# Optimization experiments

Measured on AMD Instinct MI355X. Metric: run time of the kernel, lower is better.

The kernel has to match this reference:

```python
import jax, jax.numpy as jnp
import numpy as np

B, N_IN, N_H, N_OUT = 128, 256, 256, 256


def _bimul(W, X):
    # MatrixBiMul: bilinear map W X W^T, W: [out, in], X: [b, in, in] -> [b, out, out]
    return jnp.einsum('oi,bij,qj->boq', W, X, W)


def setup_inputs() -> dict:
    key = jax.random.key(0)
    ks = jax.random.split(key, 12)
    s_in = 1.0 / np.sqrt(N_IN)
    s_h = 1.0 / np.sqrt(N_H)
    return {
        'input': jax.random.normal(ks[0], (B, N_IN, N_IN), jnp.float32),
        'hidden': jax.random.normal(ks[1], (B, N_H, N_H), jnp.float32),
        'cell': jax.random.normal(ks[2], (B, N_H, N_H), jnp.float32),
        'W_fx': jax.random.normal(ks[3], (N_H, N_IN), jnp.float32) * s_in,
        'W_ix': jax.random.normal(ks[4], (N_H, N_IN), jnp.float32) * s_in,
        'W_ox': jax.random.normal(ks[5], (N_OUT, N_IN), jnp.float32) * s_in,
        'W_gx': jax.random.normal(ks[6], (N_H, N_IN), jnp.float32) * s_in,
        'W_fh': jax.random.normal(ks[7], (N_H, N_H), jnp.float32) * s_h,
        'W_ih': jax.random.normal(ks[8], (N_H, N_H), jnp.float32) * s_h,
        'W_oh': jax.random.normal(ks[9], (N_OUT, N_H), jnp.float32) * s_h,
        'W_gh': jax.random.normal(ks[10], (N_H, N_H), jnp.float32) * s_h,
        'W_oc': jax.random.normal(ks[11], (N_OUT, N_H), jnp.float32) * s_h,
    }


def reference(input, hidden, cell, W_fx, W_ix, W_ox, W_gx, W_fh, W_ih, W_oh, W_gh, W_oc):
    fgate = jax.nn.relu(_bimul(W_fx, input) + _bimul(W_fh, hidden))
    igate = jax.nn.relu(_bimul(W_ix, input) + _bimul(W_ih, hidden))
    ogate = jax.nn.relu(_bimul(W_ox, input) + _bimul(W_oh, hidden))
    ggate = jax.nn.relu(_bimul(W_gx, input) + _bimul(W_gh, hidden))
    c = fgate + cell + igate + ggate  # note: additive, as in source (not fgate*cell)
    h = ogate + jax.nn.relu(_bimul(W_oc, c))
    return (h, c)
```

## Files before the change

### kernel.cpp

```cpp
#include <hip/hip_runtime.h>

typedef __bf16 bf16x8 __attribute__((ext_vector_type(8)));
typedef float f32x4 __attribute__((ext_vector_type(4)));

__device__ __forceinline__ unsigned short f2bf(float f) {
    unsigned int u = __builtin_bit_cast(unsigned int, f);
    u += 0x7fff + ((u >> 16) & 1);
    return (unsigned short)(u >> 16);
}

__device__ __forceinline__ void stage_pair(
    const unsigned short* __restrict__ Ap, int lda,
    const unsigned short* __restrict__ Bp, int ldb,
    unsigned short* lds, int k0, int tid)
{
#pragma unroll
    for (int it = 0; it < 4; ++it) {
        int li = it * 256 + tid;
        int row = li >> 3;
        int sc = ((li & 7) ^ (row & 7)) * 8;
        __builtin_amdgcn_global_load_lds(
            (const __attribute__((address_space(1))) void*)(Ap + (long)row * lda + k0 + sc),
            (__attribute__((address_space(3))) void*)&lds[li * 8], 16, 0, 0);
        __builtin_amdgcn_global_load_lds(
            (const __attribute__((address_space(1))) void*)(Bp + (long)row * ldb + k0 + sc),
            (__attribute__((address_space(3))) void*)&lds[8192 + li * 8], 16, 0, 0);
    }
}

__device__ __forceinline__ void stage_one(
    const unsigned short* __restrict__ Ap, int lda,
    unsigned short* buf, int k0, int tid)
{
#pragma unroll
    for (int it = 0; it < 4; ++it) {
        int li = it * 256 + tid;
        int row = li >> 3;
        int sc = ((li & 7) ^ (row & 7)) * 8;
        __builtin_amdgcn_global_load_lds(
            (const __attribute__((address_space(1))) void*)(Ap + (long)row * lda + k0 + sc),
            (__attribute__((address_space(3))) void*)&buf[li * 8], 16, 0, 0);
    }
}

__device__ __forceinline__ void compute_tile(
    const unsigned short* lds, int lane, int wm, int wn, f32x4 (&acc)[4][4])
{
#pragma unroll
    for (int kk = 0; kk < 2; ++kk) {
        const int cl = kk * 4 + (lane >> 4);
        bf16x8 af[4], bfr[4];
#pragma unroll
        for (int m = 0; m < 4; ++m) {
            int row = wm + m * 16 + (lane & 15);
            af[m] = *(const bf16x8*)&lds[row * 64 + ((cl ^ (row & 7)) * 8)];
        }
#pragma unroll
        for (int n = 0; n < 4; ++n) {
            int row = wn + n * 16 + (lane & 15);
            bfr[n] = *(const bf16x8*)&lds[8192 + row * 64 + ((cl ^ (row & 7)) * 8)];
        }
#pragma unroll
        for (int m = 0; m < 4; ++m)
#pragma unroll
            for (int n = 0; n < 4; ++n)
                acc[m][n] = __builtin_amdgcn_mfma_f32_16x16x32_bf16(af[m], bfr[n], acc[m][n], 0, 0, 0);
    }
}

__device__ __forceinline__ void compute_bsc(
    const unsigned short* bufA, const unsigned short* Sc, int k0,
    int lane, int wm, int wn, f32x4 (&acc)[4][4])
{
#pragma unroll
    for (int kk = 0; kk < 2; ++kk) {
        const int cl = kk * 4 + (lane >> 4);
        bf16x8 af[4], bfr[4];
#pragma unroll
        for (int m = 0; m < 4; ++m) {
            int row = wm + m * 16 + (lane & 15);
            af[m] = *(const bf16x8*)&bufA[row * 64 + ((cl ^ (row & 7)) * 8)];
        }
#pragma unroll
        for (int n = 0; n < 4; ++n) {
            int row = wn + n * 16 + (lane & 15);
            bfr[n] = *(const bf16x8*)&Sc[row * 256 + k0 + ((cl ^ (row & 7)) * 8)];
        }
#pragma unroll
        for (int m = 0; m < 4; ++m)
#pragma unroll
            for (int n = 0; n < 4; ++n)
                acc[m][n] = __builtin_amdgcn_mfma_f32_16x16x32_bf16(af[m], bfr[n], acc[m][n], 0, 0, 0);
    }
}

__global__ __launch_bounds__(256)
void cvt_all(const float* __restrict__ X, const float* __restrict__ H,
             unsigned short* __restrict__ XHb,
             const float* __restrict__ fx, const float* __restrict__ ix,
             const float* __restrict__ ox, const float* __restrict__ gx,
             const float* __restrict__ fh, const float* __restrict__ ih,
             const float* __restrict__ oh, const float* __restrict__ gh,
             const float* __restrict__ oc,
             unsigned short* __restrict__ Wcat, unsigned short* __restrict__ Wocb)
{
    int bid = blockIdx.x;
    if (bid < 8192) {
        long e = ((long)bid * 256 + threadIdx.x) * 8;
        const float* s = (e < 8388608) ? (X + e) : (H + (e - 8388608));
        float4 a = *(const float4*)s;
        float4 c = *(const float4*)(s + 4);
        uint4 uv;
        uv.x = (unsigned)f2bf(a.x) | ((unsigned)f2bf(a.y) << 16);
        uv.y = (unsigned)f2bf(a.z) | ((unsigned)f2bf(a.w) << 16);
        uv.z = (unsigned)f2bf(c.x) | ((unsigned)f2bf(c.y) << 16);
        uv.w = (unsigned)f2bf(c.z) | ((unsigned)f2bf(c.w) << 16);
        *(uint4*)&XHb[e] = uv;
    } else {
        int idx = (bid - 8192) * 256 + threadIdx.x;
        if (idx < 524288) {
            int g = idx >> 17;
            int rem = idx & 131071;
            int q = rem >> 9;
            int j = rem & 511;
            const float* xs = (g == 0) ? fx : (g == 1) ? ix : (g == 2) ? ox : gx;
            const float* hs = (g == 0) ? fh : (g == 1) ? ih : (g == 2) ? oh : gh;
            float v = (j < 256) ? xs[q * 256 + j] : hs[q * 256 + (j - 256)];
            Wcat[idx] = f2bf(v);
        } else if (idx < 589824) {
            int k = idx - 524288;
            Wocb[k] = f2bf(oc[k]);
        }
    }
}

__global__ __launch_bounds__(256)
void gemm_s1(const unsigned short* __restrict__ Wcat,
             const unsigned short* __restrict__ XHb,
             unsigned short* __restrict__ Tcat)
{
    __shared__ alignas(16) unsigned short lds[16384];

    const int tid = threadIdx.x;
    const int lane = tid & 63;
    const int w = tid >> 6;

    int d = blockIdx.x + 4 * blockIdx.y + 512 * blockIdx.z;
    int swz = (d & 7) * 512 + (d >> 3);
    const int x = swz & 3;
    const int b = (swz >> 2) & 127;
    const int gz = swz >> 9;
    const int g = gz >> 1, hf = gz & 1;
    const int tq = (x >> 1) * 128;
    const int ti = (x & 1) * 128;
    const int wm = (w >> 1) * 64;
    const int wn = (w & 1) * 64;

    const unsigned short* Ap = Wcat + (long)g * 131072 + (long)tq * 512 + hf * 256;
    const unsigned short* Bp = XHb + (long)hf * 8388608 + (long)b * 65536 + (long)ti * 256;

    f32x4 acc[4][4];
#pragma unroll
    for (int m = 0; m < 4; ++m)
#pragma unroll
        for (int n = 0; n < 4; ++n)
            acc[m][n] = (f32x4){0.f, 0.f, 0.f, 0.f};

#pragma unroll
    for (int t = 0; t < 4; ++t) {
        if (t > 0) __syncthreads();
        stage_pair(Ap, 512, Bp, 256, lds, t * 64, tid);
        __syncthreads();
        compute_tile(lds, lane, wm, wn, acc);
    }

    unsigned short* Cb = Tcat + (long)g * 16777216 + (long)b * 131072 + hf * 256;
    const int r0 = (lane >> 4) * 4;
    const int c0 = lane & 15;
#pragma unroll
    for (int m = 0; m < 4; ++m)
#pragma unroll
        for (int n = 0; n < 4; ++n)
#pragma unroll
            for (int r = 0; r < 4; ++r) {
                int row = tq + wm + m * 16 + r0 + r;
                int col = ti + wn + n * 16 + c0;
                Cb[(long)row * 512 + col] = f2bf(acc[m][n][r]);
            }
}

__global__ __launch_bounds__(256)
void gemm_gateB(const unsigned short* __restrict__ Tcat,
                const unsigned short* __restrict__ Wcat,
                const float* __restrict__ cell,
                float* __restrict__ out_c, float* __restrict__ out_h,
                unsigned short* __restrict__ cb16)
{
    __shared__ alignas(16) unsigned short lds[32768];

    const int tid = threadIdx.x;
    const int lane = tid & 63;
    const int w = tid >> 6;

    int orig = blockIdx.x + 4 * blockIdx.y;
    int swz = (orig & 7) * 64 + (orig >> 3);
    const int x = swz & 3;
    const int b = swz >> 2;
    const int to = (x >> 1) * 128;
    const int tq = (x & 1) * 128;
    const int wm = (w >> 1) * 64;
    const int wn = (w & 1) * 64;

    f32x4 accc[4][4], acc[4][4];
#pragma unroll
    for (int m = 0; m < 4; ++m)
#pragma unroll
        for (int n = 0; n < 4; ++n) {
            accc[m][n] = (f32x4){0.f, 0.f, 0.f, 0.f};
            acc[m][n] = (f32x4){0.f, 0.f, 0.f, 0.f};
        }

    {
        const unsigned short* Ap0 = Wcat + (long)to * 512;
        const unsigned short* Bp0 = Tcat + (long)b * 131072 + (long)tq * 512;
        stage_pair(Ap0, 512, Bp0, 512, lds, 0, tid);
    }
    for (int u = 0; u < 32; ++u) {
        __syncthreads();
        if (u + 1 < 32) {
            int s = (u + 1) >> 3;
            int gv = s ^ (s >> 1);
            const unsigned short* Ap = Wcat + (long)gv * 131072 + (long)to * 512;
            const unsigned short* Bp = Tcat + (long)gv * 16777216 + (long)b * 131072 + (long)tq * 512;
            stage_pair(Ap, 512, Bp, 512, lds + ((u + 1) & 1) * 16384, ((u + 1) & 7) * 64, tid);
        }
        compute_tile(lds + (u & 1) * 16384, lane, wm, wn, acc);
        if ((u & 7) == 7 && u != 31) {
#pragma unroll
            for (int m = 0; m < 4; ++m)
#pragma unroll
                for (int n = 0; n < 4; ++n)
#pragma unroll
                    for (int r = 0; r < 4; ++r) {
                        float v = acc[m][n][r];
                        accc[m][n][r] += (v > 0.f ? v : 0.f);
                        acc[m][n][r] = 0.f;
                    }
        }
    }

    const float* cb = cell + (long)b * 65536;
    float* co = out_c + (long)b * 65536;
    float* ho = out_h + (long)b * 65536;
    unsigned short* cbo = cb16 + (long)b * 65536;
    const int r0 = (lane >> 4) * 4;
    const int c0 = lane & 15;
#pragma unroll
    for (int m = 0; m < 4; ++m)
#pragma unroll
        for (int n = 0; n < 4; ++n)
#pragma unroll
            for (int r = 0; r < 4; ++r) {
                int row = to + wm + m * 16 + r0 + r;
                int col = tq + wn + n * 16 + c0;
                long idx = (long)row * 256 + col;
                float cv = accc[m][n][r] + cb[idx];
                co[idx] = cv;
                cbo[idx] = f2bf(cv);
                float v = acc[m][n][r];
                ho[idx] = (v > 0.f ? v : 0.f);
            }
}

__global__ __launch_bounds__(256)
void gemm_woc(const unsigned short* __restrict__ Wocb,
              const unsigned short* __restrict__ cb16,
              float* __restrict__ out_h)
{
    __shared__ alignas(16) unsigned short stg[32768];
    __shared__ alignas(16) unsigned short Sc[32768];

    const int tid = threadIdx.x;
    const int lane = tid & 63;
    const int w = tid >> 6;

    int orig = blockIdx.x + 2 * blockIdx.y;
    int swz = (orig & 7) * 32 + (orig >> 3);
    const int b = swz >> 1;
    const int tq = (swz & 1) * 128;
    const int wm = (w >> 1) * 64;
    const int wn = (w & 1) * 64;
    const int r0 = (lane >> 4) * 4;
    const int c0 = lane & 15;

#pragma unroll
    for (int t2 = 0; t2 < 2; ++t2) {
        const unsigned short* Ap = Wocb + (long)tq * 256;
        const unsigned short* Bp = cb16 + (long)b * 65536 + (long)(t2 * 128) * 256;

        f32x4 acc[4][4];
#pragma unroll
        for (int m = 0; m < 4; ++m)
#pragma unroll
            for (int n = 0; n < 4; ++n)
                acc[m][n] = (f32x4){0.f, 0.f, 0.f, 0.f};

        stage_pair(Ap, 256, Bp, 256, stg, 0, tid);
#pragma unroll
        for (int t = 0; t < 4; ++t) {
            __syncthreads();
            if (t + 1 < 4)
                stage_pair(Ap, 256, Bp, 256, stg + ((t + 1) & 1) * 16384, (t + 1) * 64, tid);
            compute_tile(stg + (t & 1) * 16384, lane, wm, wn, acc);
        }
#pragma unroll
        for (int m = 0; m < 4; ++m)
#pragma unroll
            for (int n = 0; n < 4; ++n)
#pragma unroll
                for (int r = 0; r < 4; ++r) {
                    int qrow = wm + m * 16 + r0 + r;
                    int icol = t2 * 128 + wn + n * 16 + c0;
                    int addr = qrow * 256 + (icol & ~63)
                             + ((((icol >> 3) & 7) ^ (qrow & 7)) * 8) + (icol & 7);
                    Sc[addr] = f2bf(acc[m][n][r]);
                }
    }

    float* ho = out_h + (long)b * 65536;
#pragma unroll
    for (int ot = 0; ot < 2; ++ot) {
        const unsigned short* Ap = Wocb + (long)(ot * 128) * 256;

        f32x4 acc[4][4];
#pragma unroll
        for (int m = 0; m < 4; ++m)
#pragma unroll
            for (int n = 0; n < 4; ++n)
                acc[m][n] = (f32x4){0.f, 0.f, 0.f, 0.f};

        stage_one(Ap, 256, stg, 0, tid);
#pragma unroll
        for (int t = 0; t < 4; ++t) {
            __syncthreads();
            if (t + 1 < 4)
                stage_one(Ap, 256, stg + ((t + 1) & 1) * 16384, (t + 1) * 64, tid);
            compute_bsc(stg + (t & 1) * 16384, Sc, t * 64, lane, wm, wn, acc);
        }
#pragma unroll
        for (int m = 0; m < 4; ++m)
#pragma unroll
            for (int n = 0; n < 4; ++n)
#pragma unroll
                for (int r = 0; r < 4; ++r) {
                    int orow = ot * 128 + wm + m * 16 + r0 + r;
                    int qcol = tq + wn + n * 16 + c0;
                    long idx = (long)orow * 256 + qcol;
                    float v = acc[m][n][r];
                    ho[idx] += (v > 0.f ? v : 0.f);
                }
    }
}

extern "C" void kernel_launch(void* const* d_in, const int* in_sizes, int n_in,
                              void* d_out, int out_size, void* d_ws, size_t ws_size,
                              hipStream_t stream)
{
    (void)in_sizes; (void)n_in; (void)out_size; (void)ws_size;

    const float* X    = (const float*)d_in[0];
    const float* H    = (const float*)d_in[1];
    const float* cell = (const float*)d_in[2];
    const float* Wxp[4] = {(const float*)d_in[3], (const float*)d_in[4],
                           (const float*)d_in[5], (const float*)d_in[6]};
    const float* Whp[4] = {(const float*)d_in[7], (const float*)d_in[8],
                           (const float*)d_in[9], (const float*)d_in[10]};
    const float* Wocf = (const float*)d_in[11];

    float* out_h = (float*)d_out;
    float* out_c = out_h + 8388608;

    unsigned short* ws   = (unsigned short*)d_ws;
    unsigned short* XHb  = ws;
    unsigned short* Wcat = ws + 16777216;
    unsigned short* Wocb = ws + 17301504;
    unsigned short* Tcat = ws + 17367040;
    unsigned short* cb16 = ws + 84475904;

    cvt_all<<<dim3(10496), 256, 0, stream>>>(X, H, XHb,
                                             Wxp[0], Wxp[1], Wxp[2], Wxp[3],
                                             Whp[0], Whp[1], Whp[2], Whp[3],
                                             Wocf, Wcat, Wocb);
    gemm_s1<<<dim3(4, 128, 8), 256, 0, stream>>>(Wcat, XHb, Tcat);
    gemm_gateB<<<dim3(4, 128), 256, 0, stream>>>(Tcat, Wcat, cell, out_c, out_h, cb16);
    gemm_woc<<<dim3(2, 128), 256, 0, stream>>>(Wocb, cb16, out_h);
}
```

Before: 171.5 us.

## Fuse fp32-to-bf16 conversion of input/hidden into first-stage GEMM loads

The standalone pass that converted input and hidden to a bf16 workspace is removed. The first-stage GEMM now reads fp32 activations directly into registers, prefetches the next K-slice while the current one is computed, converts to bf16 and writes swizzled tiles to LDS. This removes a full fp32 read plus bf16 write and reread of the activations. In exchange, each activation tile is reloaded in fp32 by every block that uses it (the four gates and both output row halves), which doubles bytes per reload and adds register pressure from the prefetch buffers.

```diff
diff --git a/kernel.cpp b/kernel.cpp
--- a/kernel.cpp
+++ b/kernel.cpp
@@ -95,49 +95,33 @@
 }
 
 __global__ __launch_bounds__(256)
-void cvt_all(const float* __restrict__ X, const float* __restrict__ H,
-             unsigned short* __restrict__ XHb,
-             const float* __restrict__ fx, const float* __restrict__ ix,
-             const float* __restrict__ ox, const float* __restrict__ gx,
-             const float* __restrict__ fh, const float* __restrict__ ih,
-             const float* __restrict__ oh, const float* __restrict__ gh,
-             const float* __restrict__ oc,
-             unsigned short* __restrict__ Wcat, unsigned short* __restrict__ Wocb)
-{
-    int bid = blockIdx.x;
-    if (bid < 8192) {
-        long e = ((long)bid * 256 + threadIdx.x) * 8;
-        const float* s = (e < 8388608) ? (X + e) : (H + (e - 8388608));
-        float4 a = *(const float4*)s;
-        float4 c = *(const float4*)(s + 4);
-        uint4 uv;
-        uv.x = (unsigned)f2bf(a.x) | ((unsigned)f2bf(a.y) << 16);
-        uv.y = (unsigned)f2bf(a.z) | ((unsigned)f2bf(a.w) << 16);
-        uv.z = (unsigned)f2bf(c.x) | ((unsigned)f2bf(c.y) << 16);
-        uv.w = (unsigned)f2bf(c.z) | ((unsigned)f2bf(c.w) << 16);
-        *(uint4*)&XHb[e] = uv;
-    } else {
-        int idx = (bid - 8192) * 256 + threadIdx.x;
-        if (idx < 524288) {
-            int g = idx >> 17;
-            int rem = idx & 131071;
-            int q = rem >> 9;
-            int j = rem & 511;
-            const float* xs = (g == 0) ? fx : (g == 1) ? ix : (g == 2) ? ox : gx;
-            const float* hs = (g == 0) ? fh : (g == 1) ? ih : (g == 2) ? oh : gh;
-            float v = (j < 256) ? xs[q * 256 + j] : hs[q * 256 + (j - 256)];
-            Wcat[idx] = f2bf(v);
-        } else if (idx < 589824) {
-            int k = idx - 524288;
-            Wocb[k] = f2bf(oc[k]);
-        }
+void cvt_w(const float* __restrict__ fx, const float* __restrict__ ix,
+           const float* __restrict__ ox, const float* __restrict__ gx,
+           const float* __restrict__ fh, const float* __restrict__ ih,
+           const float* __restrict__ oh, const float* __restrict__ gh,
+           const float* __restrict__ oc,
+           unsigned short* __restrict__ Wcat, unsigned short* __restrict__ Wocb)
+{
+    int idx = blockIdx.x * 256 + threadIdx.x;
+    if (idx < 524288) {
+        int g = idx >> 17;
+        int rem = idx & 131071;
+        int q = rem >> 9;
+        int j = rem & 511;
+        const float* xs = (g == 0) ? fx : (g == 1) ? ix : (g == 2) ? ox : gx;
+        const float* hs = (g == 0) ? fh : (g == 1) ? ih : (g == 2) ? oh : gh;
+        float v = (j < 256) ? xs[q * 256 + j] : hs[q * 256 + (j - 256)];
+        Wcat[idx] = f2bf(v);
+    } else if (idx < 589824) {
+        int k = idx - 524288;
+        Wocb[k] = f2bf(oc[k]);
     }
 }
 
 __global__ __launch_bounds__(256)
-void gemm_s1(const unsigned short* __restrict__ Wcat,
-             const unsigned short* __restrict__ XHb,
-             unsigned short* __restrict__ Tcat)
+void gemm_s1f(const unsigned short* __restrict__ Wcat,
+              const float* __restrict__ X, const float* __restrict__ H,
+              unsigned short* __restrict__ Tcat)
 {
     __shared__ alignas(16) unsigned short lds[16384];
 
@@ -157,7 +141,7 @@
     const int wn = (w & 1) * 64;
 
     const unsigned short* Ap = Wcat + (long)g * 131072 + (long)tq * 512 + hf * 256;
-    const unsigned short* Bp = XHb + (long)hf * 8388608 + (long)b * 65536 + (long)ti * 256;
+    const float* Bf = (hf ? H : X) + (long)b * 65536 + (long)ti * 256;
 
     f32x4 acc[4][4];
 #pragma unroll
@@ -166,11 +150,54 @@
         for (int n = 0; n < 4; ++n)
             acc[m][n] = (f32x4){0.f, 0.f, 0.f, 0.f};
 
+    float4 pre[4][2];
+#pragma unroll
+    for (int it = 0; it < 4; ++it) {
+        int li = it * 256 + tid;
+        int row = li >> 3;
+        int ck = li & 7;
+        const float* ga = Bf + (long)row * 256 + ck * 8;
+        pre[it][0] = *(const float4*)ga;
+        pre[it][1] = *(const float4*)(ga + 4);
+    }
+
 #pragma unroll
     for (int t = 0; t < 4; ++t) {
         if (t > 0) __syncthreads();
-        stage_pair(Ap, 512, Bp, 256, lds, t * 64, tid);
+#pragma unroll
+        for (int it = 0; it < 4; ++it) {
+            int li = it * 256 + tid;
+            int row = li >> 3;
+            int sc = ((li & 7) ^ (row & 7)) * 8;
+            __builtin_amdgcn_global_load_lds(
+                (const __attribute__((address_space(1))) void*)(Ap + (long)row * 512 + t * 64 + sc),
+                (__attribute__((address_space(3))) void*)&lds[li * 8], 16, 0, 0);
+        }
+#pragma unroll
+        for (int it = 0; it < 4; ++it) {
+            int li = it * 256 + tid;
+            int row = li >> 3;
+            int ck = li & 7;
+            const float* pf = (const float*)&pre[it][0];
+            uint4 uv;
+            uv.x = (unsigned)f2bf(pf[0]) | ((unsigned)f2bf(pf[1]) << 16);
+            uv.y = (unsigned)f2bf(pf[2]) | ((unsigned)f2bf(pf[3]) << 16);
+            uv.z = (unsigned)f2bf(pf[4]) | ((unsigned)f2bf(pf[5]) << 16);
+            uv.w = (unsigned)f2bf(pf[6]) | ((unsigned)f2bf(pf[7]) << 16);
+            *(uint4*)&lds[8192 + row * 64 + ((ck ^ (row & 7)) * 8)] = uv;
+        }
         __syncthreads();
+        if (t < 3) {
+#pragma unroll
+            for (int it = 0; it < 4; ++it) {
+                int li = it * 256 + tid;
+                int row = li >> 3;
+                int ck = li & 7;
+                const float* ga = Bf + (long)row * 256 + (t + 1) * 64 + ck * 8;
+                pre[it][0] = *(const float4*)ga;
+                pre[it][1] = *(const float4*)(ga + 4);
+            }
+        }
         compute_tile(lds, lane, wm, wn, acc);
     }
 
@@ -381,17 +408,15 @@
     float* out_c = out_h + 8388608;
 
     unsigned short* ws   = (unsigned short*)d_ws;
-    unsigned short* XHb  = ws;
-    unsigned short* Wcat = ws + 16777216;
-    unsigned short* Wocb = ws + 17301504;
-    unsigned short* Tcat = ws + 17367040;
-    unsigned short* cb16 = ws + 84475904;
-
-    cvt_all<<<dim3(10496), 256, 0, stream>>>(X, H, XHb,
-                                             Wxp[0], Wxp[1], Wxp[2], Wxp[3],
-                                             Whp[0], Whp[1], Whp[2], Whp[3],
-                                             Wocf, Wcat, Wocb);
-    gemm_s1<<<dim3(4, 128, 8), 256, 0, stream>>>(Wcat, XHb, Tcat);
+    unsigned short* Wcat = ws;
+    unsigned short* Wocb = ws + 524288;
+    unsigned short* Tcat = ws + 589824;
+    unsigned short* cb16 = ws + 67698688;
+
+    cvt_w<<<dim3(2304), 256, 0, stream>>>(Wxp[0], Wxp[1], Wxp[2], Wxp[3],
+                                          Whp[0], Whp[1], Whp[2], Whp[3],
+                                          Wocf, Wcat, Wocb);
+    gemm_s1f<<<dim3(4, 128, 8), 256, 0, stream>>>(Wcat, X, H, Tcat);
     gemm_gateB<<<dim3(4, 128), 256, 0, stream>>>(Tcat, Wcat, cell, out_c, out_h, cb16);
     gemm_woc<<<dim3(2, 128), 256, 0, stream>>>(Wocb, cb16, out_h);
 }
```

After: 215.9 us. 25.9% more time.

## Rewrite gate GEMM with 512-thread 128x256 tiles and triple-buffered split-stage pipeline

Applied to the files above, without the earlier changes.

The gate-combining GEMM now uses 8 waves per block covering a 128x256 output tile, so each W tile is loaded once per batch instead of twice. The staging moves to a three-buffer ring with a two-step prefetch distance, split into two parts placed around a mid-iteration barrier, and uses explicit vmcnt waits in place of full syncthreads. MFMA issue is wrapped in raised scheduling priority. The aim is to hide global-to-LDS latency and cut redundant A loads. In exchange the block needs more LDS (144KB) and has half as many blocks, which lowers occupancy.

```diff
diff --git a/kernel.cpp b/kernel.cpp
--- a/kernel.cpp
+++ b/kernel.cpp
@@ -92,6 +92,24 @@
             for (int n = 0; n < 4; ++n)
                 acc[m][n] = __builtin_amdgcn_mfma_f32_16x16x32_bf16(af[m], bfr[n], acc[m][n], 0, 0, 0);
     }
+}
+
+__device__ __forceinline__ void midbar() {
+    __builtin_amdgcn_sched_barrier(0);
+    __builtin_amdgcn_s_barrier();
+    __builtin_amdgcn_sched_barrier(0);
+}
+__device__ __forceinline__ void endbar6() {
+    asm volatile("s_waitcnt vmcnt(6)" ::: "memory");
+    __builtin_amdgcn_sched_barrier(0);
+    __builtin_amdgcn_s_barrier();
+    __builtin_amdgcn_sched_barrier(0);
+}
+__device__ __forceinline__ void endbar0() {
+    asm volatile("s_waitcnt vmcnt(0)" ::: "memory");
+    __builtin_amdgcn_sched_barrier(0);
+    __builtin_amdgcn_s_barrier();
+    __builtin_amdgcn_sched_barrier(0);
 }
 
 __global__ __launch_bounds__(256)
@@ -189,27 +207,28 @@
             }
 }
 
-__global__ __launch_bounds__(256)
-void gemm_gateB(const unsigned short* __restrict__ Tcat,
-                const unsigned short* __restrict__ Wcat,
-                const float* __restrict__ cell,
-                float* __restrict__ out_c, float* __restrict__ out_h,
-                unsigned short* __restrict__ cb16)
-{
-    __shared__ alignas(16) unsigned short lds[32768];
+__global__ __launch_bounds__(512)
+void gemm_gateB8(const unsigned short* __restrict__ Tcat,
+                 const unsigned short* __restrict__ Wcat,
+                 const float* __restrict__ cell,
+                 float* __restrict__ out_c, float* __restrict__ out_h,
+                 unsigned short* __restrict__ cb16)
+{
+    __shared__ alignas(16) unsigned short lds[73728];
 
     const int tid = threadIdx.x;
     const int lane = tid & 63;
     const int w = tid >> 6;
 
-    int orig = blockIdx.x + 4 * blockIdx.y;
-    int swz = (orig & 7) * 64 + (orig >> 3);
-    const int x = swz & 3;
-    const int b = swz >> 2;
-    const int to = (x >> 1) * 128;
-    const int tq = (x & 1) * 128;
-    const int wm = (w >> 1) * 64;
-    const int wn = (w & 1) * 64;
+    int orig = blockIdx.x + 2 * blockIdx.y;
+    int swz = (orig & 7) * 32 + (orig >> 3);
+    const int b = swz >> 1;
+    const int to = (swz & 1) * 128;
+    const int wm = (w >> 2) * 64;
+    const int wn = (w & 3) * 64;
+
+    const unsigned short* Ab = Wcat + (long)to * 512;
+    const unsigned short* Bb = Tcat + (long)b * 131072;
 
     f32x4 accc[4][4], acc[4][4];
 #pragma unroll
@@ -220,21 +239,77 @@
             acc[m][n] = (f32x4){0.f, 0.f, 0.f, 0.f};
         }
 
-    {
-        const unsigned short* Ap0 = Wcat + (long)to * 512;
-        const unsigned short* Bp0 = Tcat + (long)b * 131072 + (long)tq * 512;
-        stage_pair(Ap0, 512, Bp0, 512, lds, 0, tid);
-    }
+    auto stage = [&](int u, int part) {
+        int s = u >> 3;
+        int gv = s ^ (s >> 1);
+        int k0 = (u & 7) * 64;
+        const unsigned short* Ap = Ab + (long)gv * 131072;
+        const unsigned short* Bp = Bb + (long)gv * 16777216;
+        unsigned short* buf = lds + (u % 3) * 24576;
+        if (part == 0) {
+#pragma unroll
+            for (int it = 0; it < 2; ++it) {
+                int li = it * 512 + tid;
+                int row = li >> 3;
+                int sc = ((li & 7) ^ (row & 7)) * 8;
+                __builtin_amdgcn_global_load_lds(
+                    (const __attribute__((address_space(1))) void*)(Ap + (long)row * 512 + k0 + sc),
+                    (__attribute__((address_space(3))) void*)&buf[li * 8], 16, 0, 0);
+            }
+            {
+                int li = tid;
+                int row = li >> 3;
+                int sc = ((li & 7) ^ (row & 7)) * 8;
+                __builtin_amdgcn_global_load_lds(
+                    (const __attribute__((address_space(1))) void*)(Bp + (long)row * 512 + k0 + sc),
+                    (__attribute__((address_space(3))) void*)&buf[8192 + li * 8], 16, 0, 0);
+            }
+        } else {
+#pragma unroll
+            for (int it = 1; it < 4; ++it) {
+                int li = it * 512 + tid;
+                int row = li >> 3;
+                int sc = ((li & 7) ^ (row & 7)) * 8;
+                __builtin_amdgcn_global_load_lds(
+                    (const __attribute__((address_space(1))) void*)(Bp + (long)row * 512 + k0 + sc),
+                    (__attribute__((address_space(3))) void*)&buf[8192 + li * 8], 16, 0, 0);
+            }
+        }
+    };
+
+    auto chalf = [&](const unsigned short* buf, int kk) {
+        const int cl = kk * 4 + (lane >> 4);
+        bf16x8 af[4], bfr[4];
+#pragma unroll
+        for (int m = 0; m < 4; ++m) {
+            int row = wm + m * 16 + (lane & 15);
+            af[m] = *(const bf16x8*)&buf[row * 64 + ((cl ^ (row & 7)) * 8)];
+        }
+#pragma unroll
+        for (int n = 0; n < 4; ++n) {
+            int row = wn + n * 16 + (lane & 15);
+            bfr[n] = *(const bf16x8*)&buf[8192 + row * 64 + ((cl ^ (row & 7)) * 8)];
+        }
+        __builtin_amdgcn_s_setprio(1);
+#pragma unroll
+        for (int m = 0; m < 4; ++m)
+#pragma unroll
+            for (int n = 0; n < 4; ++n)
+                acc[m][n] = __builtin_amdgcn_mfma_f32_16x16x32_bf16(af[m], bfr[n], acc[m][n], 0, 0, 0);
+        __builtin_amdgcn_s_setprio(0);
+    };
+
+    stage(0, 0); stage(0, 1);
+    stage(1, 0); stage(1, 1);
+    endbar6();
+
     for (int u = 0; u < 32; ++u) {
-        __syncthreads();
-        if (u + 1 < 32) {
-            int s = (u + 1) >> 3;
-            int gv = s ^ (s >> 1);
-            const unsigned short* Ap = Wcat + (long)gv * 131072 + (long)to * 512;
-            const unsigned short* Bp = Tcat + (long)gv * 16777216 + (long)b * 131072 + (long)tq * 512;
-            stage_pair(Ap, 512, Bp, 512, lds + ((u + 1) & 1) * 16384, ((u + 1) & 7) * 64, tid);
-        }
-        compute_tile(lds + (u & 1) * 16384, lane, wm, wn, acc);
+        const unsigned short* cur = lds + (u % 3) * 24576;
+        if (u + 2 < 32) stage(u + 2, 0);
+        chalf(cur, 0);
+        midbar();
+        if (u + 2 < 32) stage(u + 2, 1);
+        chalf(cur, 1);
         if ((u & 7) == 7 && u != 31) {
 #pragma unroll
             for (int m = 0; m < 4; ++m)
@@ -247,6 +322,7 @@
                         acc[m][n][r] = 0.f;
                     }
         }
+        if (u < 30) endbar6(); else endbar0();
     }
 
     const float* cb = cell + (long)b * 65536;
@@ -262,7 +338,7 @@
 #pragma unroll
             for (int r = 0; r < 4; ++r) {
                 int row = to + wm + m * 16 + r0 + r;
-                int col = tq + wn + n * 16 + c0;
+                int col = wn + n * 16 + c0;
                 long idx = (long)row * 256 + col;
                 float cv = accc[m][n][r] + cb[idx];
                 co[idx] = cv;
@@ -392,6 +468,6 @@
                                              Whp[0], Whp[1], Whp[2], Whp[3],
                                              Wocf, Wcat, Wocb);
     gemm_s1<<<dim3(4, 128, 8), 256, 0, stream>>>(Wcat, XHb, Tcat);
-    gemm_gateB<<<dim3(4, 128), 256, 0, stream>>>(Tcat, Wcat, cell, out_c, out_h, cb16);
+    gemm_gateB8<<<dim3(2, 128), 512, 0, stream>>>(Tcat, Wcat, cell, out_c, out_h, cb16);
     gemm_woc<<<dim3(2, 128), 256, 0, stream>>>(Wocb, cb16, out_h);
 }
```

Measured after the change: 171.2 us. No clear change (-0.2%).
